# Optimization experiments

Measured on AMD Instinct MI355X. Metric: run time of the kernel, lower is better.

## Reference

```python
import jax, jax.numpy as jnp
import numpy as np

N_NODES = 100000
HIDDEN = 128
N_EDGES = 1000000


def setup_inputs() -> dict:
    key = jax.random.key(0)
    k1, k2, k3, k4 = jax.random.split(key, 4)
    node_embeddings = jax.random.normal(k1, (N_NODES, HIDDEN), dtype=jnp.float32)
    legal_moves = jax.random.randint(k2, (2, N_EDGES), 0, N_NODES, dtype=jnp.int64)
    # Linear(2H -> H) and Linear(H -> 1) weights (stored input-major for x @ W)
    W1 = jax.random.normal(k3, (2 * HIDDEN, HIDDEN), dtype=jnp.float32) * (1.0 / np.sqrt(2 * HIDDEN))
    b1 = jnp.zeros((HIDDEN,), dtype=jnp.float32)
    W2 = jax.random.normal(k4, (HIDDEN, 1), dtype=jnp.float32) * (1.0 / np.sqrt(HIDDEN))
    b2 = jnp.zeros((1,), dtype=jnp.float32)
    return {
        "node_embeddings": node_embeddings,
        "legal_moves": legal_moves,
        "W1": W1,
        "b1": b1,
        "W2": W2,
        "b2": b2,
    }


def reference(node_embeddings, legal_moves, W1, b1, W2, b2):
    sources = legal_moves[0]
    targets = legal_moves[1]
    h_source = node_embeddings[sources]          # [E, H]
    h_target = node_embeddings[targets]          # [E, H]
    move_features = jnp.concatenate([h_source, h_target], axis=-1)  # [E, 2H]
    hidden = jax.nn.relu(move_features @ W1 + b1)                   # [E, H]
    logits = (hidden @ W2 + b2).squeeze(-1)                         # [E]
    probs = jax.nn.softmax(logits, axis=-1)
    return probs
```

## Files before the change

### kernel.cpp

```cpp
#include <hip/hip_runtime.h>
#include <hip/hip_bf16.h>
#include <hip/hip_fp16.h>
#include <stdint.h>

#define NNODES 100000
#define HID 128
#define NEDGES 1000000
#define NEBLOCKS 15625

typedef __attribute__((ext_vector_type(8))) short short8;
typedef __attribute__((ext_vector_type(4))) float floatx4;
typedef _Float16 f16x2 __attribute__((ext_vector_type(2)));
typedef _Float16 f16x4 __attribute__((ext_vector_type(4)));
typedef _Float16 f16x8 __attribute__((ext_vector_type(8)));

__global__ __launch_bounds__(256) void pack_b_kernel(
    const float* __restrict__ W1, _Float16* __restrict__ Bf) {
  const int t = blockIdx.x * 256 + threadIdx.x;
  const int lane = t & 63;
  const int ks = (t >> 6) & 3;
  const int ct = t >> 8;
  const int n = ct * 16 + (lane & 15);
  const int kb = ks * 32 + ((lane >> 4) * 8);
  f16x8 h;
#pragma unroll
  for (int j = 0; j < 8; ++j) {
    const int k = kb + j;
    const float v = (n < HID) ? W1[(size_t)k * HID + n]
                              : W1[(size_t)(HID + k) * HID + (n - HID)];
    h[j] = (_Float16)v;
  }
  *(f16x8*)(Bf + (size_t)t * 8) = h;
}

__global__ __launch_bounds__(256) void project_kernel(
    const float* __restrict__ emb, const _Float16* __restrict__ Bf,
    __half* __restrict__ P) {
  __shared__ __align__(16) char smem[64 * 264 * 2];
  _Float16* As = (_Float16*)smem;
  __half* Co = (__half*)smem;

  const int t = threadIdx.x;
  const int lane = t & 63;
  const int w = t >> 6;
  const int l16 = lane & 15;
  const int q = lane >> 4;
  const int row0 = blockIdx.x * 64;

  {
    const int r_base = t >> 5;
    const int col = (t & 31) * 4;
#pragma unroll
    for (int i = 0; i < 8; ++i) {
      int grow = row0 + r_base + i * 8;
      if (grow >= NNODES) grow = NNODES - 1;
      const floatx4 v = *(const floatx4*)(emb + (size_t)grow * HID + col);
      f16x4 h;
      h[0] = (_Float16)v.x; h[1] = (_Float16)v.y;
      h[2] = (_Float16)v.z; h[3] = (_Float16)v.w;
      *(f16x4*)&As[(r_base + i * 8) * 136 + col] = h;
    }
  }
  __syncthreads();

  floatx4 acc[4][4] = {};
#pragma unroll
  for (int ks = 0; ks < 4; ++ks) {
    f16x8 bh[4];
#pragma unroll
    for (int ct = 0; ct < 4; ++ct) {
      const size_t idx = (size_t)(((w * 4 + ct) * 4 + ks) * 64 + lane) * 8;
      bh[ct] = *(const f16x8*)(Bf + idx);
    }
    f16x8 ah[4];
#pragma unroll
    for (int rt = 0; rt < 4; ++rt)
      ah[rt] = *(const f16x8*)&As[(rt * 16 + l16) * 136 + ks * 32 + q * 8];
#pragma unroll
    for (int rt = 0; rt < 4; ++rt)
#pragma unroll
      for (int ct = 0; ct < 4; ++ct)
        acc[rt][ct] = __builtin_amdgcn_mfma_f32_16x16x32_f16(ah[rt], bh[ct], acc[rt][ct], 0, 0, 0);
  }

  __syncthreads();
#pragma unroll
  for (int rt = 0; rt < 4; ++rt)
#pragma unroll
    for (int ct = 0; ct < 4; ++ct)
#pragma unroll
      for (int r = 0; r < 4; ++r) {
        const int row = rt * 16 + q * 4 + r;
        const int col = w * 64 + ct * 16 + l16;
        Co[row * 264 + col] = __float2half(acc[rt][ct][r]);
      }
  __syncthreads();
#pragma unroll
  for (int i = 0; i < 8; ++i) {
    const int chunk = t + i * 256;
    const int row = chunk >> 5;
    const int cx = chunk & 31;
    if (row0 + row < NNODES) {
      const floatx4 v = *(const floatx4*)&Co[row * 264 + cx * 8];
      *(floatx4*)(P + (size_t)(row0 + row) * 256 + cx * 8) = v;
    }
  }
}

__global__ __launch_bounds__(256) void edge_kernel(
    const __half* __restrict__ P, const int* __restrict__ lm,
    const float* __restrict__ b1, const float* __restrict__ W2,
    const float* __restrict__ b2, float* __restrict__ explog,
    float* __restrict__ partials) {
  const int lane = threadIdx.x & 63;
  const int wid = threadIdx.x >> 6;
  const int g = lane >> 4;
  const int l16 = lane & 15;
  const int c = l16 * 8;

  f16x2 b1h[4], w2h[4];
  {
    const floatx4 b1a = *(const floatx4*)(b1 + c);
    const floatx4 b1b = *(const floatx4*)(b1 + c + 4);
    const floatx4 w2a = *(const floatx4*)(W2 + c);
    const floatx4 w2b = *(const floatx4*)(W2 + c + 4);
    b1h[0] = f16x2{(_Float16)b1a.x, (_Float16)b1a.y};
    b1h[1] = f16x2{(_Float16)b1a.z, (_Float16)b1a.w};
    b1h[2] = f16x2{(_Float16)b1b.x, (_Float16)b1b.y};
    b1h[3] = f16x2{(_Float16)b1b.z, (_Float16)b1b.w};
    w2h[0] = f16x2{(_Float16)w2a.x, (_Float16)w2a.y};
    w2h[1] = f16x2{(_Float16)w2a.z, (_Float16)w2a.w};
    w2h[2] = f16x2{(_Float16)w2b.x, (_Float16)w2b.y};
    w2h[3] = f16x2{(_Float16)w2b.z, (_Float16)w2b.w};
  }
  const f16x2 z2 = {(_Float16)0.f, (_Float16)0.f};
  const float b2v = b2[0];

  const int e0 = (blockIdx.x * 4 + wid) * 16;

  uint4 rs[4], rt_[4];
#pragma unroll
  for (int j = 0; j < 4; ++j) {
    const int ej = e0 + j * 4 + g;
    const int src = lm[ej];
    const int tgt = lm[NEDGES + ej];
    rs[j]  = *(const uint4*)(P + (size_t)src * 256 + c);
    rt_[j] = *(const uint4*)(P + (size_t)tgt * 256 + 128 + c);
  }
  float lsum = 0.f;
#pragma unroll
  for (int j = 0; j < 4; ++j) {
    float p = 0.f;
    const unsigned su[4] = {rs[j].x, rs[j].y, rs[j].z, rs[j].w};
    const unsigned tu[4] = {rt_[j].x, rt_[j].y, rt_[j].z, rt_[j].w};
#pragma unroll
    for (int h = 0; h < 4; ++h) {
      const f16x2 s = __builtin_bit_cast(f16x2, su[h]);
      const f16x2 tt = __builtin_bit_cast(f16x2, tu[h]);
      const f16x2 a = __builtin_elementwise_max(s + tt + b1h[h], z2);
      p = __builtin_amdgcn_fdot2(a, w2h[h], p, false);
    }
    p += __shfl_xor(p, 8, 64);
    p += __shfl_xor(p, 4, 64);
    p += __shfl_xor(p, 2, 64);
    p += __shfl_xor(p, 1, 64);
    if (l16 == j) {
      const float ev = __expf(p + b2v);
      explog[e0 + j * 4 + g] = ev;
      lsum += ev;
    }
  }

#pragma unroll
  for (int off = 32; off >= 1; off >>= 1) lsum += __shfl_xor(lsum, off, 64);
  __shared__ float wsums[4];
  if (lane == 0) wsums[wid] = lsum;
  __syncthreads();
  if (threadIdx.x == 0)
    partials[blockIdx.x] = wsums[0] + wsums[1] + wsums[2] + wsums[3];
}

__global__ __launch_bounds__(256) void reduce_kernel(
    const float* __restrict__ partials, float* __restrict__ accum) {
  float s = 0.f;
  for (int i = threadIdx.x; i < 3906; i += 256) {
    const floatx4 v = *(const floatx4*)(partials + i * 4);
    s += (v.x + v.y) + (v.z + v.w);
  }
  if (threadIdx.x == 0) s += partials[15624];
#pragma unroll
  for (int off = 32; off >= 1; off >>= 1) s += __shfl_xor(s, off, 64);
  __shared__ float ws_[4];
  if ((threadIdx.x & 63) == 0) ws_[threadIdx.x >> 6] = s;
  __syncthreads();
  if (threadIdx.x == 0) accum[0] = ws_[0] + ws_[1] + ws_[2] + ws_[3];
}

__global__ __launch_bounds__(256) void norm_kernel(
    const float* __restrict__ explog, const float* __restrict__ sum_accum,
    float* __restrict__ out) {
  const float inv = 1.0f / *sum_accum;
  const int i = (blockIdx.x * 256 + threadIdx.x) * 4;
  if (i < NEDGES) {
    floatx4 v = *(const floatx4*)(explog + i);
    v.x *= inv; v.y *= inv; v.z *= inv; v.w *= inv;
    *(floatx4*)(out + i) = v;
  }
}

extern "C" void kernel_launch(void* const* d_in, const int* in_sizes, int n_in,
                              void* d_out, int out_size, void* d_ws, size_t ws_size,
                              hipStream_t stream) {
  const float* emb = (const float*)d_in[0];
  const int*   lm  = (const int*)d_in[1];
  const float* W1  = (const float*)d_in[2];
  const float* b1  = (const float*)d_in[3];
  const float* W2  = (const float*)d_in[4];
  const float* b2  = (const float*)d_in[5];
  float* out = (float*)d_out;

  char* ws = (char*)d_ws;
  __half* P       = (__half*)ws;
  float* accum    = (float*)(ws + 51200000);
  float* explog   = (float*)(ws + 51200256);
  _Float16* Bf    = (_Float16*)(ws + 55200256);
  float* partials = (float*)(ws + 55265792);

  pack_b_kernel<<<16, 256, 0, stream>>>(W1, Bf);
  project_kernel<<<1563, 256, 0, stream>>>(emb, Bf, P);
  edge_kernel<<<NEBLOCKS, 256, 0, stream>>>(P, lm, b1, W2, b2, explog, partials);
  reduce_kernel<<<1, 256, 0, stream>>>(partials, accum);
  norm_kernel<<<977, 256, 0, stream>>>(explog, accum, out);
}
```

Before: 182.8 us.

## Quantize projected node features to int8 with per-half-row scales

The projection kernel now stores each node's precomputed source and target projections as uint8 with a per-half-row absmax scale instead of fp16. This halves the bytes gathered per edge in the edge kernel. The edge kernel dequantizes in fp32 using the scales and does the ReLU and dot in fp32 FMAs. In exchange it adds quantization error to the logits, an extra scattered scale load per endpoint, and more per-element ALU work.

Result: faster. 158.0 us (-13.5%).

```diff
diff --git a/kernel.cpp b/kernel.cpp
--- a/kernel.cpp
+++ b/kernel.cpp
@@ -2,13 +2,13 @@
 #include <hip/hip_bf16.h>
 #include <hip/hip_fp16.h>
 #include <stdint.h>
+#include <math.h>
 
 #define NNODES 100000
 #define HID 128
 #define NEDGES 1000000
 #define NEBLOCKS 15625
 
-typedef __attribute__((ext_vector_type(8))) short short8;
 typedef __attribute__((ext_vector_type(4))) float floatx4;
 typedef _Float16 f16x2 __attribute__((ext_vector_type(2)));
 typedef _Float16 f16x4 __attribute__((ext_vector_type(4)));
@@ -35,7 +35,7 @@
 
 __global__ __launch_bounds__(256) void project_kernel(
     const float* __restrict__ emb, const _Float16* __restrict__ Bf,
-    __half* __restrict__ P) {
+    uint8_t* __restrict__ P, float* __restrict__ scalesInv) {
   __shared__ __align__(16) char smem[64 * 264 * 2];
   _Float16* As = (_Float16*)smem;
   __half* Co = (__half*)smem;
@@ -96,19 +96,48 @@
       }
   __syncthreads();
 #pragma unroll
-  for (int i = 0; i < 8; ++i) {
+  for (int i = 0; i < 4; ++i) {
     const int chunk = t + i * 256;
-    const int row = chunk >> 5;
-    const int cx = chunk & 31;
-    if (row0 + row < NNODES) {
-      const floatx4 v = *(const floatx4*)&Co[row * 264 + cx * 8];
-      *(floatx4*)(P + (size_t)(row0 + row) * 256 + cx * 8) = v;
+    const int row = chunk >> 4;
+    const int cx = chunk & 15;
+    const int half = cx >> 3;
+    const f16x8 v0 = *(const f16x8*)&Co[row * 264 + cx * 16];
+    const f16x8 v1 = *(const f16x8*)&Co[row * 264 + cx * 16 + 8];
+    float f[16];
+#pragma unroll
+    for (int k = 0; k < 8; ++k) { f[k] = (float)v0[k]; f[8 + k] = (float)v1[k]; }
+    float m = 0.f;
+#pragma unroll
+    for (int k = 0; k < 16; ++k) m = fmaxf(m, fabsf(f[k]));
+    m = fmaxf(m, __shfl_xor(m, 1, 64));
+    m = fmaxf(m, __shfl_xor(m, 2, 64));
+    m = fmaxf(m, __shfl_xor(m, 4, 64));
+    m = fmaxf(m, 1e-20f);
+    const float qs = 127.0f / m;
+    const int grow = row0 + row;
+    if (grow < NNODES) {
+      if ((cx & 7) == 0) scalesInv[2 * grow + half] = m * (1.0f / 127.0f);
+      unsigned d[4];
+#pragma unroll
+      for (int dw = 0; dw < 4; ++dw) {
+        unsigned acc_b = 0;
+#pragma unroll
+        for (int b = 0; b < 4; ++b) {
+          int qv = (int)rintf(f[dw * 4 + b] * qs) + 128;
+          qv = qv < 0 ? 0 : (qv > 255 ? 255 : qv);
+          acc_b |= ((unsigned)qv) << (8 * b);
+        }
+        d[dw] = acc_b;
+      }
+      uint4 o; o.x = d[0]; o.y = d[1]; o.z = d[2]; o.w = d[3];
+      *(uint4*)(P + (size_t)grow * 256 + cx * 16) = o;
     }
   }
 }
 
 __global__ __launch_bounds__(256) void edge_kernel(
-    const __half* __restrict__ P, const int* __restrict__ lm,
+    const uint8_t* __restrict__ P, const float* __restrict__ scalesInv,
+    const int* __restrict__ lm,
     const float* __restrict__ b1, const float* __restrict__ W2,
     const float* __restrict__ b2, float* __restrict__ explog,
     float* __restrict__ partials) {
@@ -118,47 +147,51 @@
   const int l16 = lane & 15;
   const int c = l16 * 8;
 
-  f16x2 b1h[4], w2h[4];
+  float b1f[8], w2f[8];
   {
     const floatx4 b1a = *(const floatx4*)(b1 + c);
     const floatx4 b1b = *(const floatx4*)(b1 + c + 4);
     const floatx4 w2a = *(const floatx4*)(W2 + c);
     const floatx4 w2b = *(const floatx4*)(W2 + c + 4);
-    b1h[0] = f16x2{(_Float16)b1a.x, (_Float16)b1a.y};
-    b1h[1] = f16x2{(_Float16)b1a.z, (_Float16)b1a.w};
-    b1h[2] = f16x2{(_Float16)b1b.x, (_Float16)b1b.y};
-    b1h[3] = f16x2{(_Float16)b1b.z, (_Float16)b1b.w};
-    w2h[0] = f16x2{(_Float16)w2a.x, (_Float16)w2a.y};
-    w2h[1] = f16x2{(_Float16)w2a.z, (_Float16)w2a.w};
-    w2h[2] = f16x2{(_Float16)w2b.x, (_Float16)w2b.y};
-    w2h[3] = f16x2{(_Float16)w2b.z, (_Float16)w2b.w};
-  }
-  const f16x2 z2 = {(_Float16)0.f, (_Float16)0.f};
+    b1f[0] = b1a.x; b1f[1] = b1a.y; b1f[2] = b1a.z; b1f[3] = b1a.w;
+    b1f[4] = b1b.x; b1f[5] = b1b.y; b1f[6] = b1b.z; b1f[7] = b1b.w;
+    w2f[0] = w2a.x; w2f[1] = w2a.y; w2f[2] = w2a.z; w2f[3] = w2a.w;
+    w2f[4] = w2b.x; w2f[5] = w2b.y; w2f[6] = w2b.z; w2f[7] = w2b.w;
+  }
   const float b2v = b2[0];
 
   const int e0 = (blockIdx.x * 4 + wid) * 16;
 
-  uint4 rs[4], rt_[4];
+  uint2 rs[4], rt_[4];
+  float ssv[4], stv[4];
 #pragma unroll
   for (int j = 0; j < 4; ++j) {
     const int ej = e0 + j * 4 + g;
     const int src = lm[ej];
     const int tgt = lm[NEDGES + ej];
-    rs[j]  = *(const uint4*)(P + (size_t)src * 256 + c);
-    rt_[j] = *(const uint4*)(P + (size_t)tgt * 256 + 128 + c);
+    rs[j]  = *(const uint2*)(P + (size_t)src * 256 + c);
+    rt_[j] = *(const uint2*)(P + (size_t)tgt * 256 + 128 + c);
+    ssv[j] = scalesInv[2 * src];
+    stv[j] = scalesInv[2 * tgt + 1];
   }
   float lsum = 0.f;
 #pragma unroll
   for (int j = 0; j < 4; ++j) {
+    const float si = ssv[j], ti = stv[j];
+    const float cb = -128.0f * (si + ti);
     float p = 0.f;
-    const unsigned su[4] = {rs[j].x, rs[j].y, rs[j].z, rs[j].w};
-    const unsigned tu[4] = {rt_[j].x, rt_[j].y, rt_[j].z, rt_[j].w};
-#pragma unroll
-    for (int h = 0; h < 4; ++h) {
-      const f16x2 s = __builtin_bit_cast(f16x2, su[h]);
-      const f16x2 tt = __builtin_bit_cast(f16x2, tu[h]);
-      const f16x2 a = __builtin_elementwise_max(s + tt + b1h[h], z2);
-      p = __builtin_amdgcn_fdot2(a, w2h[h], p, false);
+    const unsigned su[2] = {rs[j].x, rs[j].y};
+    const unsigned tu[2] = {rt_[j].x, rt_[j].y};
+#pragma unroll
+    for (int w = 0; w < 2; ++w) {
+#pragma unroll
+      for (int b = 0; b < 4; ++b) {
+        const float sf = (float)((su[w] >> (8 * b)) & 0xffu);
+        const float tf = (float)((tu[w] >> (8 * b)) & 0xffu);
+        const int ch = w * 4 + b;
+        const float pre = fmaf(sf, si, fmaf(tf, ti, b1f[ch] + cb));
+        p = fmaf(fmaxf(pre, 0.f), w2f[ch], p);
+      }
     }
     p += __shfl_xor(p, 8, 64);
     p += __shfl_xor(p, 4, 64);
@@ -220,15 +253,16 @@
   float* out = (float*)d_out;
 
   char* ws = (char*)d_ws;
-  __half* P       = (__half*)ws;
-  float* accum    = (float*)(ws + 51200000);
-  float* explog   = (float*)(ws + 51200256);
-  _Float16* Bf    = (_Float16*)(ws + 55200256);
-  float* partials = (float*)(ws + 55265792);
+  uint8_t* P      = (uint8_t*)ws;
+  float* accum    = (float*)(ws + 25600000);
+  float* explog   = (float*)(ws + 25600256);
+  _Float16* Bf    = (_Float16*)(ws + 29600256);
+  float* partials = (float*)(ws + 29665792);
+  float* scalesInv = (float*)(ws + 29728512);
 
   pack_b_kernel<<<16, 256, 0, stream>>>(W1, Bf);
-  project_kernel<<<1563, 256, 0, stream>>>(emb, Bf, P);
-  edge_kernel<<<NEBLOCKS, 256, 0, stream>>>(P, lm, b1, W2, b2, explog, partials);
+  project_kernel<<<1563, 256, 0, stream>>>(emb, Bf, P, scalesInv);
+  edge_kernel<<<NEBLOCKS, 256, 0, stream>>>(P, scalesInv, lm, b1, W2, b2, explog, partials);
   reduce_kernel<<<1, 256, 0, stream>>>(partials, accum);
   norm_kernel<<<977, 256, 0, stream>>>(explog, accum, out);
 }
```
